# Kernel optimization log

Measured on AMD Instinct MI355X. Metric: run time of the kernel, lower is better.

## Reference

```python
import jax, jax.numpy as jnp
import numpy as np

# config constants (match init_kwargs)
EPS = 1e-6
LAYER_TEMP = 1.0
MIN_GATE = 0.1
MAX_GATE = 0.9
MAX_STATE_NORM = 10.0
EVIDENCE_SCALE = 256.0
STATE_DECAY = 0.0

B, L, E, H, G, R = 2, 32, 256, 4096, 16, 64


def _normalize(x, axis=-1):
    # torch F.normalize: x / max(||x||, eps)
    n = jnp.linalg.norm(x, axis=axis, keepdims=True)
    return x / jnp.maximum(n, EPS)


def setup_inputs() -> dict:
    key = jax.random.key(0)
    ks = jax.random.split(key, 8)
    return {
        "state": jax.random.normal(ks[0], (B, R), jnp.float32),
        "evicted_k": jax.random.normal(ks[1], (B, L, E, H), jnp.float32) * 0.02,
        "evicted_v": jax.random.normal(ks[2], (B, L, E, H), jnp.float32) * 0.02,
        "Wq": jax.random.normal(ks[3], (R, H), jnp.float32) * 0.02,
        "Wk": jax.random.normal(ks[4], (R, H), jnp.float32) * 0.02,
        "Wv": jax.random.normal(ks[5], (R, H), jnp.float32) * 0.02,
        "global_q": jax.random.normal(ks[6], (G, H), jnp.float32) * 0.02,
        "layer_query": jax.random.normal(ks[7], (R,), jnp.float32) * 0.02,
        "evicted_tokens_per_layer": 256,
    }


def reference(state, evicted_k, evicted_v, Wq, Wk, Wv, global_q, layer_query,
              evicted_tokens_per_layer):
    rank = Wq.shape[0]
    inv_sqrt_r = 1.0 / jnp.sqrt(jnp.float32(rank))

    # ---- layer attention over L (use_layer_attention=True) ----
    layer_k = evicted_k.mean(axis=2)                                  # [B,L,H]
    layer_scores = jnp.einsum('blh,rh,r->bl', layer_k, Wk, layer_query)
    layer_scores = layer_scores * (inv_sqrt_r / LAYER_TEMP)
    layer_w = jax.nn.softmax(layer_scores, axis=1)                    # [B,L]
    ek = jnp.einsum('bleh,bl->beh', evicted_k, layer_w)               # [B,E,H]
    ev = jnp.einsum('bleh,bl->beh', evicted_v, layer_w)               # [B,E,H]

    # ---- low-rank cross attention: global queries over evicted tokens ----
    q = global_q @ Wq.T                                               # [G,R]
    k = jnp.einsum('beh,rh->ber', ek, Wk)                             # [B,E,R]
    v = jnp.einsum('beh,rh->ber', ev, Wv)                             # [B,E,R]
    scores = jnp.einsum('gr,ber->bge', q, k) * inv_sqrt_r             # [B,G,E]
    attn = jax.nn.softmax(scores, axis=-1)
    context = jnp.einsum('bge,ber->bgr', attn, v)                     # [B,G,R]
    s_new = context.mean(axis=1)                                      # [B,R]

    # ---- gated state update (detach_prev_state=True) ----
    prev = jax.lax.stop_gradient(state)
    sim = jnp.sum(_normalize(prev) * _normalize(s_new), axis=-1)
    sim = jnp.clip(sim, -1.0, 1.0)
    gate = MIN_GATE + (MAX_GATE - MIN_GATE) * 0.5 * (sim + 1.0)
    evidence = jnp.minimum(1.0, jnp.float32(evicted_tokens_per_layer) / EVIDENCE_SCALE)
    gate = (gate * evidence)[:, None]                                 # [B,1]

    updated = (1.0 - STATE_DECAY) * (1.0 - gate) * prev + gate * s_new

    # clamp state norm to max_state_norm
    n = jnp.linalg.norm(updated, axis=-1, keepdims=True)
    updated = updated * jnp.minimum(1.0, MAX_STATE_NORM / jnp.maximum(n, EPS))
    return updated
```

## Files before the change

kernel.cpp:

```cpp
#include <hip/hip_runtime.h>
#include <hip/hip_bf16.h>
#include <stdint.h>

#define BB 2
#define LL 32
#define EE 256
#define HH 4096
#define GG 16
#define RR 64

typedef __bf16 bf16x8 __attribute__((ext_vector_type(8)));
typedef float f32x4 __attribute__((ext_vector_type(4)));

__device__ inline void async16(const void* g, void* l) {
    __builtin_amdgcn_global_load_lds((const __attribute__((address_space(1))) uint32_t*)g,
                                     (__attribute__((address_space(3))) uint32_t*)l, 16, 0, 0);
}

__device__ inline bf16x8 cvt8(f32x4 a, f32x4 b) {
    bf16x8 r;
    r[0] = (__bf16)a[0]; r[1] = (__bf16)a[1]; r[2] = (__bf16)a[2]; r[3] = (__bf16)a[3];
    r[4] = (__bf16)b[0]; r[5] = (__bf16)b[1]; r[6] = (__bf16)b[2]; r[7] = (__bf16)b[3];
    return r;
}

__global__ __launch_bounds__(256) void prep_kernel(
    const float* __restrict__ Wk, const float* __restrict__ Wv,
    __hip_bfloat16* __restrict__ Bfrag, float* __restrict__ scores)
{
    const int tid = blockIdx.x * 256 + threadIdx.x;
    const int mat = tid >> 15;
    const int kq  = (tid >> 6) & 511;
    const int r   = tid & 63;
    const float* W = mat ? Wv : Wk;
    const float* src = W + (size_t)r * HH + kq * 8;
    f32x4 a = *(const f32x4*)src;
    f32x4 b = *(const f32x4*)(src + 4);
    *(bf16x8*)((__bf16*)Bfrag + (size_t)tid * 8) = cvt8(a, b);
    if (blockIdx.x == 0 && threadIdx.x < BB * LL) scores[threadIdx.x] = 0.f;
}

__global__ __launch_bounds__(256, 4) void proj_kernel(
    const float* __restrict__ ek, const float* __restrict__ ev,
    const __hip_bfloat16* __restrict__ Bfrag, const float* __restrict__ lq,
    __hip_bfloat16* __restrict__ kpart, __hip_bfloat16* __restrict__ vpart,
    float* __restrict__ scores)
{
    __shared__ __align__(16) uint8_t sm[49152];
    uint8_t* smA = sm;
    uint8_t* smB = sm + 24576;

    const int blk  = blockIdx.x;
    const int bl   = blk >> 3;
    const int e0   = (blk & 7) * 32;
    const int t    = threadIdx.x;
    const int w    = t >> 6;
    const int lane = t & 63;
    const int n    = lane & 15;
    const int q    = lane >> 4;
    const int mat  = w >> 1;
    const int mt   = w & 1;

    const int row_l = lane >> 3;
    const int aswz  = ((lane & 7) ^ row_l) << 4;
    const char* astage = (const char*)((w & 1) ? ev : ek)
        + ((size_t)(bl * EE + e0 + row_l) * HH) * 4 + aswz;
    const char* bstage = (const char*)Bfrag + ((w & 1) ? (size_t)512 * 1024 : (size_t)0)
        + (size_t)lane * 16;
    uint8_t* adst0 = smA + (w & 1) * 4096;
    uint8_t* bdst0 = smB + (w & 1) * 4096;
    const bool isA = (w < 2);

    auto stage = [&](int cc, int sb) {
        if (isA) {
            const char* g = astage + (size_t)cc * 128;
            uint8_t* d = adst0 + sb * 8192;
#pragma unroll
            for (int p = 0; p < 4; ++p)
                async16(g + (size_t)p * (8 * HH * 4), d + p * 1024);
        } else {
            const char* g = bstage + (size_t)cc * 4096;
            uint8_t* d = bdst0 + sb * 8192;
#pragma unroll
            for (int i = 0; i < 4; ++i)
                async16(g + i * 1024, d + i * 1024);
        }
    };

    f32x4 acc[4] = {};
    const int m = mt * 16 + n;
    const uint8_t* arow0 = smA + mat * 4096 + m * 128;
    const int sA0 = ((2 * q) ^ (n & 7)) << 4;
    const int sA1 = ((2 * q + 1) ^ (n & 7)) << 4;
    const uint8_t* brow0 = smB + mat * 4096 + q * 1024 + n * 16;

    stage(0, 0);
    stage(1, 1);

    int cb = 0;
    for (int c = 0; c < 128; ++c) {
        asm volatile("s_waitcnt vmcnt(4)" ::: "memory");
        __builtin_amdgcn_s_barrier();
        asm volatile("" ::: "memory");

        stage((c + 2) & 127, cb >= 1 ? cb - 1 : 2);

        const uint8_t* arow = arow0 + cb * 8192;
        f32x4 a0 = *(const f32x4*)(arow + sA0);
        f32x4 a1 = *(const f32x4*)(arow + sA1);
        bf16x8 af = cvt8(a0, a1);
        const uint8_t* brow = brow0 + cb * 8192;
#pragma unroll
        for (int nt = 0; nt < 4; ++nt) {
            bf16x8 bv = *(const bf16x8*)(brow + nt * 256);
            acc[nt] = __builtin_amdgcn_mfma_f32_16x16x32_bf16(af, bv, acc[nt], 0, 0, 0);
        }
        asm volatile("" ::: "memory");
        cb = (cb == 2) ? 0 : cb + 1;
    }

    __hip_bfloat16* outp = (mat == 0) ? kpart : vpart;
    float lqv[4];
    if (mat == 0) {
#pragma unroll
        for (int nt = 0; nt < 4; ++nt) lqv[nt] = lq[nt * 16 + n];
    }
    float sc = 0.f;
#pragma unroll
    for (int nt = 0; nt < 4; ++nt)
#pragma unroll
        for (int reg = 0; reg < 4; ++reg) {
            const int e_row = e0 + mt * 16 + q * 4 + reg;
            outp[((size_t)bl * EE + e_row) * RR + nt * 16 + n] = __float2bfloat16(acc[nt][reg]);
            if (mat == 0) sc += acc[nt][reg] * lqv[nt];
        }
    if (mat == 0) {
#pragma unroll
        for (int off = 32; off > 0; off >>= 1) sc += __shfl_down(sc, off, 64);
        if (lane == 0) atomicAdd(&scores[bl], sc);
    }
    asm volatile("s_waitcnt vmcnt(0)" ::: "memory");
}

__global__ __launch_bounds__(256) void kber_kernel(
    const __hip_bfloat16* __restrict__ kpart, const __hip_bfloat16* __restrict__ vpart,
    const float* __restrict__ scores,
    float* __restrict__ k2, float* __restrict__ v2)
{
    const int blk = blockIdx.x;
    const int b   = blk >> 4;
    const int mat = (blk >> 3) & 1;
    const int e0  = (blk & 7) * 32;
    const int t = threadIdx.x, w = t >> 6, lane = t & 63;

    float sv = scores[b * LL + (lane & 31)] * (1.f / 2048.f);
    float mx = sv;
#pragma unroll
    for (int off = 16; off; off >>= 1) mx = fmaxf(mx, __shfl_xor(mx, off));
    float ex = __expf(sv - mx), sum = ex;
#pragma unroll
    for (int off = 16; off; off >>= 1) sum += __shfl_xor(sum, off);
    const float wgt = ex / sum;

    const int e  = e0 + w * 8 + (lane >> 3);
    const int r8 = (lane & 7) * 8;
    const __hip_bfloat16* src = mat ? vpart : kpart;
    const __bf16* base = (const __bf16*)src + ((size_t)b * LL * EE + e) * RR + r8;
    float acc[8] = {};
    for (int l = 0; l < LL; ++l) {
        const float wl = __shfl(wgt, l);
        bf16x8 v8 = *(const bf16x8*)(base + (size_t)l * EE * RR);
#pragma unroll
        for (int j = 0; j < 8; ++j) acc[j] += wl * (float)v8[j];
    }
    float* dst = (mat ? v2 : k2) + ((size_t)b * EE + e) * RR + r8;
    f32x4 o0 = {acc[0], acc[1], acc[2], acc[3]};
    f32x4 o1 = {acc[4], acc[5], acc[6], acc[7]};
    *(f32x4*)dst = o0;
    *(f32x4*)(dst + 4) = o1;
}

__global__ __launch_bounds__(256) void qproj_kernel(
    const float* __restrict__ gq, const float* __restrict__ Wq,
    float* __restrict__ q)
{
    const int g  = blockIdx.x >> 2;
    const int rq = blockIdx.x & 3;
    const int t  = threadIdx.x;
    __shared__ float red[16][256];
    __shared__ float r2[16][17];
    float s[16] = {};
    for (int i = 0; i < 4; i++) {
        const int h = i * 1024 + t * 4;
        f32x4 a = *(const f32x4*)(gq + (size_t)g * HH + h);
#pragma unroll
        for (int r = 0; r < 16; r++) {
            f32x4 wv_ = *(const f32x4*)(Wq + (size_t)(rq * 16 + r) * HH + h);
            s[r] += a[0] * wv_[0] + a[1] * wv_[1] + a[2] * wv_[2] + a[3] * wv_[3];
        }
    }
#pragma unroll
    for (int r = 0; r < 16; r++) red[r][t] = s[r];
    __syncthreads();
    {
        const int r = t >> 4, j = t & 15;
        float p = 0.f;
        for (int i = 0; i < 16; i++) p += red[r][j * 16 + i];
        r2[r][j] = p;
    }
    __syncthreads();
    if (t < 16) {
        float p = 0.f;
        for (int j = 0; j < 16; j++) p += r2[t][j];
        q[g * RR + rq * 16 + t] = p;
    }
}

__global__ __launch_bounds__(256) void final_kernel(
    const float* __restrict__ q, const float* __restrict__ k2,
    const float* __restrict__ v2, const float* __restrict__ state,
    const int* __restrict__ tokens, float* __restrict__ out)
{
    const int b = blockIdx.x;
    const int t = threadIdx.x;
    const int w = t >> 6, lane = t & 63;
    __shared__ float qs[GG * RR];
    __shared__ float ctxw[4][RR];

    for (int i = t; i < GG * RR; i += 256) qs[i] = q[i];
    __syncthreads();

    const float* kb = k2 + (size_t)b * EE * RR;
    const float* vb = v2 + (size_t)b * EE * RR;
    float ctxsum = 0.f;
#pragma unroll
    for (int gi = 0; gi < 4; ++gi) {
        const int g = w * 4 + gi;
        float sarr[4];
#pragma unroll
        for (int k = 0; k < 4; ++k) {
            const float* krow = kb + (size_t)(k * 64 + lane) * RR;
            f32x4 a = {};
#pragma unroll
            for (int r4 = 0; r4 < 16; ++r4) {
                f32x4 kv = *(const f32x4*)(krow + r4 * 4);
                f32x4 qv = *(const f32x4*)(qs + g * RR + r4 * 4);
                a += kv * qv;
            }
            sarr[k] = (a[0] + a[1] + a[2] + a[3]) * 0.125f;
        }
        float mx = fmaxf(fmaxf(sarr[0], sarr[1]), fmaxf(sarr[2], sarr[3]));
#pragma unroll
        for (int off = 32; off; off >>= 1) mx = fmaxf(mx, __shfl_xor(mx, off));
        float ps[4]; float sum = 0.f;
#pragma unroll
        for (int k = 0; k < 4; ++k) { ps[k] = __expf(sarr[k] - mx); sum += ps[k]; }
#pragma unroll
        for (int off = 32; off; off >>= 1) sum += __shfl_xor(sum, off);
        const float inv = 1.0f / sum;
        float c = 0.f;
#pragma unroll
        for (int k = 0; k < 4; ++k) {
            const float pk = ps[k] * inv;
#pragma unroll 8
            for (int e = 0; e < 64; ++e) {
                const float pe = __shfl(pk, e);
                c += pe * vb[(size_t)(k * 64 + e) * RR + lane];
            }
        }
        ctxsum += c;
    }
    ctxw[w][lane] = ctxsum;
    __syncthreads();

    if (w == 0) {
        const float snew = (ctxw[0][lane] + ctxw[1][lane] + ctxw[2][lane] + ctxw[3][lane]) * (1.0f / GG);
        const float prev = state[b * RR + lane];
        float np = prev * prev, ns = snew * snew, dp = prev * snew;
#pragma unroll
        for (int off = 32; off; off >>= 1) {
            np += __shfl_xor(np, off);
            ns += __shfl_xor(ns, off);
            dp += __shfl_xor(dp, off);
        }
        float sim = dp / (fmaxf(sqrtf(np), 1e-6f) * fmaxf(sqrtf(ns), 1e-6f));
        sim = fminf(1.0f, fmaxf(-1.0f, sim));
        float gate = 0.1f + 0.8f * 0.5f * (sim + 1.0f);
        const int tv = tokens[0];
        float tokf = (tv >= 0 && tv < (1 << 24)) ? (float)tv : __int_as_float(tv);
        gate *= fminf(1.0f, tokf * (1.0f / 256.0f));
        const float upd = (1.0f - gate) * prev + gate * snew;
        float nn = upd * upd;
#pragma unroll
        for (int off = 32; off; off >>= 1) nn += __shfl_xor(nn, off);
        const float scale = fminf(1.0f, 10.0f / fmaxf(sqrtf(nn), 1e-6f));
        out[b * RR + lane] = upd * scale;
    }
}

extern "C" void kernel_launch(void* const* d_in, const int* in_sizes, int n_in,
                              void* d_out, int out_size, void* d_ws, size_t ws_size,
                              hipStream_t stream) {
    const float* state = (const float*)d_in[0];
    const float* ek    = (const float*)d_in[1];
    const float* ev    = (const float*)d_in[2];
    const float* Wq    = (const float*)d_in[3];
    const float* Wk    = (const float*)d_in[4];
    const float* Wv    = (const float*)d_in[5];
    const float* gq    = (const float*)d_in[6];
    const float* lq    = (const float*)d_in[7];
    const int*   tok   = (const int*)d_in[8];
    float* out = (float*)d_out;

    const size_t n_part = (size_t)BB * LL * EE * RR;
    __hip_bfloat16* kpart = (__hip_bfloat16*)d_ws;
    __hip_bfloat16* vpart = kpart + n_part;
    __hip_bfloat16* Bfrag = vpart + n_part;
    float* fr      = (float*)(Bfrag + (size_t)2 * 512 * 64 * 8);
    float* scores  = fr;
    float* k2      = scores + BB * LL;
    float* v2      = k2 + (size_t)BB * EE * RR;
    float* qbuf    = v2 + (size_t)BB * EE * RR;

    prep_kernel<<<256, 256, 0, stream>>>(Wk, Wv, Bfrag, scores);
    proj_kernel<<<512, 256, 0, stream>>>(ek, ev, Bfrag, lq, kpart, vpart, scores);
    kber_kernel<<<32, 256, 0, stream>>>(kpart, vpart, scores, k2, v2);
    qproj_kernel<<<64, 256, 0, stream>>>(gq, Wq, qbuf);
    final_kernel<<<BB, 256, 0, stream>>>(qbuf, k2, v2, state, tok, out);
}
```

Measured before the change: 616.1 us.

## Fuse q projection into prep kernel and merge layer-weighting into final tail kernel

The q projection now runs as extra blocks of the prep kernel, and the per-layer softmax weighting of kpart/vpart is folded into the final kernel. The combined k2/v2 now live in shared memory rather than global buffers, which removes two kernel launches and a global round trip. The cost is that the layer reduction over all of E and L now runs in only two blocks of 256 threads. That serializes work that was previously spread over 32 blocks. Shared memory use also grows to roughly 150KB per block.

```diff
diff --git a/kernel.cpp b/kernel.cpp
--- a/kernel.cpp
+++ b/kernel.cpp
@@ -24,20 +24,57 @@
     return r;
 }
 
-__global__ __launch_bounds__(256) void prep_kernel(
+__global__ __launch_bounds__(256) void prep_q_kernel(
     const float* __restrict__ Wk, const float* __restrict__ Wv,
-    __hip_bfloat16* __restrict__ Bfrag, float* __restrict__ scores)
+    const float* __restrict__ Wq, const float* __restrict__ gq,
+    __hip_bfloat16* __restrict__ Bfrag, float* __restrict__ qbuf,
+    float* __restrict__ scores)
 {
-    const int tid = blockIdx.x * 256 + threadIdx.x;
-    const int mat = tid >> 15;
-    const int kq  = (tid >> 6) & 511;
-    const int r   = tid & 63;
-    const float* W = mat ? Wv : Wk;
-    const float* src = W + (size_t)r * HH + kq * 8;
-    f32x4 a = *(const f32x4*)src;
-    f32x4 b = *(const f32x4*)(src + 4);
-    *(bf16x8*)((__bf16*)Bfrag + (size_t)tid * 8) = cvt8(a, b);
-    if (blockIdx.x == 0 && threadIdx.x < BB * LL) scores[threadIdx.x] = 0.f;
+    __shared__ float red[16][256];
+    __shared__ float r2[16][17];
+    const int blk = blockIdx.x;
+    if (blk < 256) {
+        const int tid = blk * 256 + threadIdx.x;
+        const int mat = tid >> 15;
+        const int kq  = (tid >> 6) & 511;
+        const int r   = tid & 63;
+        const float* W = mat ? Wv : Wk;
+        const float* src = W + (size_t)r * HH + kq * 8;
+        f32x4 a = *(const f32x4*)src;
+        f32x4 b = *(const f32x4*)(src + 4);
+        *(bf16x8*)((__bf16*)Bfrag + (size_t)tid * 8) = cvt8(a, b);
+        if (blk == 0 && threadIdx.x < BB * LL) scores[threadIdx.x] = 0.f;
+        return;
+    }
+    const int qb = blk - 256;
+    const int g  = qb >> 2;
+    const int rq = qb & 3;
+    const int t  = threadIdx.x;
+    float s[16] = {};
+    for (int i = 0; i < 4; i++) {
+        const int h = i * 1024 + t * 4;
+        f32x4 a = *(const f32x4*)(gq + (size_t)g * HH + h);
+#pragma unroll
+        for (int r = 0; r < 16; r++) {
+            f32x4 wv_ = *(const f32x4*)(Wq + (size_t)(rq * 16 + r) * HH + h);
+            s[r] += a[0] * wv_[0] + a[1] * wv_[1] + a[2] * wv_[2] + a[3] * wv_[3];
+        }
+    }
+#pragma unroll
+    for (int r = 0; r < 16; r++) red[r][t] = s[r];
+    __syncthreads();
+    {
+        const int r = t >> 4, j = t & 15;
+        float p = 0.f;
+        for (int i = 0; i < 16; i++) p += red[r][j * 16 + i];
+        r2[r][j] = p;
+    }
+    __syncthreads();
+    if (t < 16) {
+        float p = 0.f;
+        for (int j = 0; j < 16; j++) p += r2[t][j];
+        qbuf[g * RR + rq * 16 + t] = p;
+    }
 }
 
 __global__ __launch_bounds__(256, 4) void proj_kernel(
@@ -142,96 +179,59 @@
     asm volatile("s_waitcnt vmcnt(0)" ::: "memory");
 }
 
-__global__ __launch_bounds__(256) void kber_kernel(
+#define K2S 68
+#define V2S 65
+__global__ __launch_bounds__(256) void tail_kernel(
     const __hip_bfloat16* __restrict__ kpart, const __hip_bfloat16* __restrict__ vpart,
-    const float* __restrict__ scores,
-    float* __restrict__ k2, float* __restrict__ v2)
+    const float* __restrict__ scores, const float* __restrict__ q,
+    const float* __restrict__ state, const int* __restrict__ tokens,
+    float* __restrict__ out)
 {
-    const int blk = blockIdx.x;
-    const int b   = blk >> 4;
-    const int mat = (blk >> 3) & 1;
-    const int e0  = (blk & 7) * 32;
-    const int t = threadIdx.x, w = t >> 6, lane = t & 63;
-
-    float sv = scores[b * LL + (lane & 31)] * (1.f / 2048.f);
-    float mx = sv;
-#pragma unroll
-    for (int off = 16; off; off >>= 1) mx = fmaxf(mx, __shfl_xor(mx, off));
-    float ex = __expf(sv - mx), sum = ex;
-#pragma unroll
-    for (int off = 16; off; off >>= 1) sum += __shfl_xor(sum, off);
-    const float wgt = ex / sum;
-
-    const int e  = e0 + w * 8 + (lane >> 3);
-    const int r8 = (lane & 7) * 8;
-    const __hip_bfloat16* src = mat ? vpart : kpart;
-    const __bf16* base = (const __bf16*)src + ((size_t)b * LL * EE + e) * RR + r8;
-    float acc[8] = {};
-    for (int l = 0; l < LL; ++l) {
-        const float wl = __shfl(wgt, l);
-        bf16x8 v8 = *(const bf16x8*)(base + (size_t)l * EE * RR);
-#pragma unroll
-        for (int j = 0; j < 8; ++j) acc[j] += wl * (float)v8[j];
-    }
-    float* dst = (mat ? v2 : k2) + ((size_t)b * EE + e) * RR + r8;
-    f32x4 o0 = {acc[0], acc[1], acc[2], acc[3]};
-    f32x4 o1 = {acc[4], acc[5], acc[6], acc[7]};
-    *(f32x4*)dst = o0;
-    *(f32x4*)(dst + 4) = o1;
-}
-
-__global__ __launch_bounds__(256) void qproj_kernel(
-    const float* __restrict__ gq, const float* __restrict__ Wq,
-    float* __restrict__ q)
-{
-    const int g  = blockIdx.x >> 2;
-    const int rq = blockIdx.x & 3;
-    const int t  = threadIdx.x;
-    __shared__ float red[16][256];
-    __shared__ float r2[16][17];
-    float s[16] = {};
-    for (int i = 0; i < 4; i++) {
-        const int h = i * 1024 + t * 4;
-        f32x4 a = *(const f32x4*)(gq + (size_t)g * HH + h);
-#pragma unroll
-        for (int r = 0; r < 16; r++) {
-            f32x4 wv_ = *(const f32x4*)(Wq + (size_t)(rq * 16 + r) * HH + h);
-            s[r] += a[0] * wv_[0] + a[1] * wv_[1] + a[2] * wv_[2] + a[3] * wv_[3];
-        }
-    }
-#pragma unroll
-    for (int r = 0; r < 16; r++) red[r][t] = s[r];
-    __syncthreads();
-    {
-        const int r = t >> 4, j = t & 15;
-        float p = 0.f;
-        for (int i = 0; i < 16; i++) p += red[r][j * 16 + i];
-        r2[r][j] = p;
-    }
-    __syncthreads();
-    if (t < 16) {
-        float p = 0.f;
-        for (int j = 0; j < 16; j++) p += r2[t][j];
-        q[g * RR + rq * 16 + t] = p;
-    }
-}
-
-__global__ __launch_bounds__(256) void final_kernel(
-    const float* __restrict__ q, const float* __restrict__ k2,
-    const float* __restrict__ v2, const float* __restrict__ state,
-    const int* __restrict__ tokens, float* __restrict__ out)
-{
+    __shared__ float k2[EE][K2S];
+    __shared__ float v2[EE][V2S];
+    __shared__ float qs[GG * RR];
+    __shared__ float pw[4][EE];
+    __shared__ float ctxw[4][RR];
+
     const int b = blockIdx.x;
     const int t = threadIdx.x;
     const int w = t >> 6, lane = t & 63;
-    __shared__ float qs[GG * RR];
-    __shared__ float ctxw[4][RR];
+
+    float sv = scores[b * LL + (lane & 31)] * (1.f / 2048.f);
+    float mx = sv;
+#pragma unroll
+    for (int off = 16; off; off >>= 1) mx = fmaxf(mx, __shfl_xor(mx, off));
+    float ex = __expf(sv - mx), sum = ex;
+#pragma unroll
+    for (int off = 16; off; off >>= 1) sum += __shfl_xor(sum, off);
+    const float wgt = ex / sum;
 
     for (int i = t; i < GG * RR; i += 256) qs[i] = q[i];
+
+    const int r8 = t & 7;
+    const int eb = t >> 3;
+#pragma unroll
+    for (int es = 0; es < 8; ++es) {
+        const int e = eb + 32 * es;
+        float ak[8] = {}, av[8] = {};
+        const __bf16* kb = (const __bf16*)kpart + ((size_t)(b * LL) * EE + e) * RR + r8 * 8;
+        const __bf16* vb = (const __bf16*)vpart + ((size_t)(b * LL) * EE + e) * RR + r8 * 8;
+#pragma unroll 4
+        for (int l = 0; l < LL; ++l) {
+            const float wl = __shfl(wgt, l);
+            bf16x8 k8 = *(const bf16x8*)(kb + (size_t)l * EE * RR);
+            bf16x8 v8 = *(const bf16x8*)(vb + (size_t)l * EE * RR);
+#pragma unroll
+            for (int j = 0; j < 8; ++j) { ak[j] += wl * (float)k8[j]; av[j] += wl * (float)v8[j]; }
+        }
+#pragma unroll
+        for (int j = 0; j < 8; ++j) {
+            k2[e][r8 * 8 + j] = ak[j];
+            v2[e][r8 * 8 + j] = av[j];
+        }
+    }
     __syncthreads();
 
-    const float* kb = k2 + (size_t)b * EE * RR;
-    const float* vb = v2 + (size_t)b * EE * RR;
     float ctxsum = 0.f;
 #pragma unroll
     for (int gi = 0; gi < 4; ++gi) {
@@ -239,35 +239,30 @@
         float sarr[4];
 #pragma unroll
         for (int k = 0; k < 4; ++k) {
-            const float* krow = kb + (size_t)(k * 64 + lane) * RR;
+            const int e = k * 64 + lane;
             f32x4 a = {};
 #pragma unroll
             for (int r4 = 0; r4 < 16; ++r4) {
-                f32x4 kv = *(const f32x4*)(krow + r4 * 4);
+                f32x4 kv = *(const f32x4*)(&k2[e][r4 * 4]);
                 f32x4 qv = *(const f32x4*)(qs + g * RR + r4 * 4);
                 a += kv * qv;
             }
             sarr[k] = (a[0] + a[1] + a[2] + a[3]) * 0.125f;
         }
-        float mx = fmaxf(fmaxf(sarr[0], sarr[1]), fmaxf(sarr[2], sarr[3]));
-#pragma unroll
-        for (int off = 32; off; off >>= 1) mx = fmaxf(mx, __shfl_xor(mx, off));
-        float ps[4]; float sum = 0.f;
-#pragma unroll
-        for (int k = 0; k < 4; ++k) { ps[k] = __expf(sarr[k] - mx); sum += ps[k]; }
-#pragma unroll
-        for (int off = 32; off; off >>= 1) sum += __shfl_xor(sum, off);
-        const float inv = 1.0f / sum;
+        float mg = fmaxf(fmaxf(sarr[0], sarr[1]), fmaxf(sarr[2], sarr[3]));
+#pragma unroll
+        for (int off = 32; off; off >>= 1) mg = fmaxf(mg, __shfl_xor(mg, off));
+        float ps[4]; float sg = 0.f;
+#pragma unroll
+        for (int k = 0; k < 4; ++k) { ps[k] = __expf(sarr[k] - mg); sg += ps[k]; }
+#pragma unroll
+        for (int off = 32; off; off >>= 1) sg += __shfl_xor(sg, off);
+        const float inv = 1.0f / sg;
+#pragma unroll
+        for (int k = 0; k < 4; ++k) pw[w][k * 64 + lane] = ps[k] * inv;
         float c = 0.f;
-#pragma unroll
-        for (int k = 0; k < 4; ++k) {
-            const float pk = ps[k] * inv;
 #pragma unroll 8
-            for (int e = 0; e < 64; ++e) {
-                const float pe = __shfl(pk, e);
-                c += pe * vb[(size_t)(k * 64 + e) * RR + lane];
-            }
-        }
+        for (int e = 0; e < EE; ++e) c += pw[w][e] * v2[e][lane];
         ctxsum += c;
     }
     ctxw[w][lane] = ctxsum;
@@ -318,13 +313,9 @@
     __hip_bfloat16* Bfrag = vpart + n_part;
     float* fr      = (float*)(Bfrag + (size_t)2 * 512 * 64 * 8);
     float* scores  = fr;
-    float* k2      = scores + BB * LL;
-    float* v2      = k2 + (size_t)BB * EE * RR;
-    float* qbuf    = v2 + (size_t)BB * EE * RR;
-
-    prep_kernel<<<256, 256, 0, stream>>>(Wk, Wv, Bfrag, scores);
+    float* qbuf    = scores + BB * LL;
+
+    prep_q_kernel<<<320, 256, 0, stream>>>(Wk, Wv, Wq, gq, Bfrag, qbuf, scores);
     proj_kernel<<<512, 256, 0, stream>>>(ek, ev, Bfrag, lq, kpart, vpart, scores);
-    kber_kernel<<<32, 256, 0, stream>>>(kpart, vpart, scores, k2, v2);
-    qproj_kernel<<<64, 256, 0, stream>>>(gq, Wq, qbuf);
-    final_kernel<<<BB, 256, 0, stream>>>(qbuf, k2, v2, state, tok, out);
-}
+    tail_kernel<<<BB, 256, 0, stream>>>(kpart, vpart, scores, qbuf, state, tok, out);
+}
```

New measurement: 589.2 us. 4.4% less time.
